# Kernel optimization log

Measured on AMD Instinct MI355X. Metric: run time of the kernel, lower is better.

## Reference

```python
import jax, jax.numpy as jnp
import numpy as np


def _upsample_bilinear_ac(img, out_h, out_w):
    # bilinear upsample with align_corners=True (matches nn.Upsample(..., align_corners=True))
    B, C, H, W = img.shape
    ys = jnp.linspace(0.0, H - 1.0, out_h)
    xs = jnp.linspace(0.0, W - 1.0, out_w)
    y0 = jnp.floor(ys).astype(jnp.int32)
    y1 = jnp.clip(y0 + 1, 0, H - 1)
    x0 = jnp.floor(xs).astype(jnp.int32)
    x1 = jnp.clip(x0 + 1, 0, W - 1)
    wy = (ys - y0).astype(img.dtype)
    wx = (xs - x0).astype(img.dtype)
    top = img[:, :, y0, :] * (1 - wy)[None, None, :, None] + img[:, :, y1, :] * wy[None, None, :, None]
    out = top[:, :, :, x0] * (1 - wx)[None, None, None, :] + top[:, :, :, x1] * wx[None, None, None, :]
    return out


def setup_inputs() -> dict:
    key = jax.random.key(0)
    ks = jax.random.split(key, 10)
    B, Cin, H, W = 4, 1024, 128, 128
    Cy, Hy, Wy = 2, 64, 64
    x = jax.random.normal(ks[0], (B, Cin, H, W), jnp.float32)
    y = jax.random.normal(ks[1], (B, Cy, Hy, Wy), jnp.float32)
    s = 0.5
    wq = jax.random.normal(ks[2], (Cy, Cy), jnp.float32) * s
    bq = jax.random.normal(ks[3], (Cy,), jnp.float32) * 0.1
    wk = jax.random.normal(ks[4], (Cy, Cy), jnp.float32) * s
    bk = jax.random.normal(ks[5], (Cy,), jnp.float32) * 0.1
    wv = jax.random.normal(ks[6], (Cy, Cy), jnp.float32) * s
    bv = jax.random.normal(ks[7], (Cy,), jnp.float32) * 0.1
    gamma = jnp.full((1,), 0.5, jnp.float32)  # torch init is 0; use 0.5 so the attention branch is active
    conv_w = jax.random.normal(ks[8], (Cy, Cin, 3, 3), jnp.float32) * (1.0 / np.sqrt(Cin * 9))
    conv_b = jnp.zeros((Cy,), jnp.float32)
    bn_scale = jnp.ones((Cy,), jnp.float32)
    bn_bias = jnp.zeros((Cy,), jnp.float32)
    bn_mean = jnp.zeros((Cy,), jnp.float32)
    bn_var = jax.random.uniform(ks[9], (Cy,), jnp.float32, 0.5, 1.5)
    return {"x": x, "y": y, "wq": wq, "bq": bq, "wk": wk, "bk": bk, "wv": wv, "bv": bv,
            "gamma": gamma, "conv_w": conv_w, "conv_b": conv_b,
            "bn_scale": bn_scale, "bn_bias": bn_bias, "bn_mean": bn_mean, "bn_var": bn_var}


def reference(x, y, wq, bq, wk, bk, wv, bv, gamma, conv_w, conv_b, bn_scale, bn_bias, bn_mean, bn_var):
    B, Cy, Hy, Wy = y.shape
    N = Hy * Wy
    h, w = x.shape[2], x.shape[3]
    # 1x1 convs on y = channel matmuls
    q = jnp.einsum('oc,bchw->bohw', wq, y) + bq[None, :, None, None]
    k = jnp.einsum('oc,bchw->bohw', wk, y) + bk[None, :, None, None]
    v = jnp.einsum('oc,bchw->bohw', wv, y) + bv[None, :, None, None]
    qf = q.reshape(B, Cy, N)
    kf = k.reshape(B, Cy, N)
    vf = v.reshape(B, Cy, N)
    # energy[b,i,j] = sum_c q[b,c,i] * k[b,c,j]; softmax over j
    energy = jnp.einsum('bci,bcj->bij', qf, kf)
    attn = jax.nn.softmax(energy, axis=-1)
    # out[b,c,i] = sum_j v[b,c,j] * attn[b,i,j]
    out = jnp.einsum('bcj,bij->bci', vf, attn).reshape(B, Cy, Hy, Wy)
    y1 = gamma * out + y
    y1_up = _upsample_bilinear_ac(y1, h, w)
    y_up = _upsample_bilinear_ac(y, h, w)
    # Conv2dBnRelu: 3x3 conv pad 1, BN (eval mode), ReLU
    xc = jax.lax.conv_general_dilated(x, conv_w, (1, 1), ((1, 1), (1, 1)),
                                      dimension_numbers=('NCHW', 'OIHW', 'NCHW'))
    xc = xc + conv_b[None, :, None, None]
    inv = (bn_scale / jnp.sqrt(bn_var + 1e-5))[None, :, None, None]
    xc = (xc - bn_mean[None, :, None, None]) * inv + bn_bias[None, :, None, None]
    xc = jax.nn.relu(xc)
    return y_up + xc * y1_up
```

## Files before the change

kernel.cpp:

```cpp
#include <hip/hip_runtime.h>

#define NATT 4096

__global__ __launch_bounds__(256) void attn_y1_kernel(
    const float* __restrict__ y,
    const float* __restrict__ wq, const float* __restrict__ bq,
    const float* __restrict__ wk, const float* __restrict__ bk,
    const float* __restrict__ wv, const float* __restrict__ bv,
    const float* __restrict__ gammaP,
    float* __restrict__ y1out)
{
    __shared__ float kv[16 * 1024];
    const int tid = threadIdx.x;
    const int blk = blockIdx.x;
    const int b   = blk >> 6;
    const int i0  = (blk & 63) << 6;
    const float* yb = y + (size_t)b * 2 * NATT;

    const float wk00 = wk[0], wk01 = wk[1], wk10 = wk[2], wk11 = wk[3];
    const float wv00 = wv[0], wv01 = wv[1], wv10 = wv[2], wv11 = wv[3];
    const float bk0 = bk[0], bk1 = bk[1], bv0 = bv[0], bv1 = bv[1];

#pragma unroll
    for (int t = 0; t < 16; ++t) {
        int j = tid + (t << 8);
        float ya  = yb[j];
        float ybv = yb[NATT + j];
        float k0 = wk00 * ya + wk01 * ybv + bk0;
        float k1 = wk10 * ya + wk11 * ybv + bk1;
        float v0 = wv00 * ya + wv01 * ybv + bv0;
        float v1 = wv10 * ya + wv11 * ybv + bv1;
        int addr = (t << 10) + (((tid + t) & 255) << 2);
        *(float4*)&kv[addr] = make_float4(k0, k1, v0, v1);
    }
    __syncthreads();

    const int jseg = tid & 15;
    const int ii   = tid >> 4;

    const float wq00 = wq[0], wq01 = wq[1], wq10 = wq[2], wq11 = wq[3];
    const float bq0 = bq[0], bq1 = bq[1];

    float q0[4], q1[4];
#pragma unroll
    for (int m = 0; m < 4; ++m) {
        int i = i0 + ii + (m << 4);
        float ya = yb[i], ybv = yb[NATT + i];
        q0[m] = wq00 * ya + wq01 * ybv + bq0;
        q1[m] = wq10 * ya + wq11 * ybv + bq1;
    }

    float s[4]  = {0.f, 0.f, 0.f, 0.f};
    float a0[4] = {0.f, 0.f, 0.f, 0.f};
    float a1[4] = {0.f, 0.f, 0.f, 0.f};
    const int base = jseg << 10;
#pragma unroll 4
    for (int jj = 0; jj < 256; ++jj) {
        float4 kvv = *(const float4*)&kv[base + (((jj + jseg) & 255) << 2)];
#pragma unroll
        for (int m = 0; m < 4; ++m) {
            float e = fmaf(q0[m], kvv.x, q1[m] * kvv.y);
            float p = __expf(e);
            s[m] += p;
            a0[m] = fmaf(p, kvv.z, a0[m]);
            a1[m] = fmaf(p, kvv.w, a1[m]);
        }
    }
#pragma unroll
    for (int d = 1; d < 16; d <<= 1) {
#pragma unroll
        for (int m = 0; m < 4; ++m) {
            s[m]  += __shfl_xor(s[m],  d, 64);
            a0[m] += __shfl_xor(a0[m], d, 64);
            a1[m] += __shfl_xor(a1[m], d, 64);
        }
    }
    if (jseg == 0) {
        float g = gammaP[0];
#pragma unroll
        for (int m = 0; m < 4; ++m) {
            int i = i0 + ii + (m << 4);
            float o0 = a0[m] / s[m];
            float o1 = a1[m] / s[m];
            y1out[(size_t)b * 2 * NATT + i]        = g * o0 + yb[i];
            y1out[(size_t)b * 2 * NATT + NATT + i] = g * o1 + yb[NATT + i];
        }
    }
}

__global__ __launch_bounds__(256) void conv_part_kernel(
    const float* __restrict__ x, const float* __restrict__ cw,
    float* __restrict__ part)
{
    const int bid = blockIdx.x;
    const int g = bid & 31;
    const int s = (bid >> 5) & 3;
    const int b = bid >> 7;
    const int tid = threadIdx.x;
    const int col = tid & 31;
    const int rg  = tid >> 5;
    const int rowbase = (s << 5) + (rg << 2);
    const int lane = tid & 63;

    const float* xp  = x + (((size_t)(b * 1024 + g * 32)) << 14) + (col << 2);
    const float* w0p = cw + (size_t)g * 32 * 9;
    const float* w1p = w0p + 9216;

    float4 acc[4][2];
#pragma unroll
    for (int i = 0; i < 4; ++i)
#pragma unroll
        for (int oc = 0; oc < 2; ++oc)
            acc[i][oc] = make_float4(0.f, 0.f, 0.f, 0.f);

    float4 cur[6], nxt[6];
    auto loadrows = [&](int c, float4* dst) {
        const float* xc = xp + ((size_t)c << 14);
#pragma unroll
        for (int k = 0; k < 6; ++k) {
            int gr  = rowbase - 1 + k;
            int grc = gr < 0 ? 0 : (gr > 127 ? 127 : gr);
            float4 v = *(const float4*)(xc + (grc << 7));
            if (gr < 0 || gr > 127) v = make_float4(0.f, 0.f, 0.f, 0.f);
            dst[k] = v;
        }
    };

    loadrows(0, cur);
#pragma unroll 1
    for (int ci = 0; ci < 32; ++ci) {
        if (ci < 31) loadrows(ci + 1, nxt);
        const float* wa = w0p + ci * 9;
        const float* wb = w1p + ci * 9;
        float W[2][9];
#pragma unroll
        for (int t = 0; t < 9; ++t) { W[0][t] = wa[t]; W[1][t] = wb[t]; }

        float lf[6], rf[6];
#pragma unroll
        for (int k = 0; k < 6; ++k) {
            float lv = __shfl(cur[k].w, (lane - 1) & 63, 64);
            float rv = __shfl(cur[k].x, (lane + 1) & 63, 64);
            lf[k] = (col == 0)  ? 0.f : lv;
            rf[k] = (col == 31) ? 0.f : rv;
        }
#pragma unroll
        for (int i = 0; i < 4; ++i) {
#pragma unroll
            for (int dr = 0; dr < 3; ++dr) {
                const int k = i + dr;
                const float f0 = lf[k],  f1 = cur[k].x, f2 = cur[k].y,
                            f3 = cur[k].z, f4 = cur[k].w, f5 = rf[k];
#pragma unroll
                for (int oc = 0; oc < 2; ++oc) {
                    const float w0 = W[oc][dr * 3 + 0];
                    const float w1 = W[oc][dr * 3 + 1];
                    const float w2 = W[oc][dr * 3 + 2];
                    acc[i][oc].x = fmaf(w0, f0, fmaf(w1, f1, fmaf(w2, f2, acc[i][oc].x)));
                    acc[i][oc].y = fmaf(w0, f1, fmaf(w1, f2, fmaf(w2, f3, acc[i][oc].y)));
                    acc[i][oc].z = fmaf(w0, f2, fmaf(w1, f3, fmaf(w2, f4, acc[i][oc].z)));
                    acc[i][oc].w = fmaf(w0, f3, fmaf(w1, f4, fmaf(w2, f5, acc[i][oc].w)));
                }
            }
        }
        if (ci < 31) {
#pragma unroll
            for (int k = 0; k < 6; ++k) cur[k] = nxt[k];
        }
    }

    float* pb = part + (((size_t)(g * 4 + b) * 2) << 14) + (col << 2);
#pragma unroll
    for (int i = 0; i < 4; ++i) {
        int orow = rowbase + i;
        *(float4*)(pb + (orow << 7))             = acc[i][0];
        *(float4*)(pb + (1 << 14) + (orow << 7)) = acc[i][1];
    }
}

__global__ __launch_bounds__(256) void combine_kernel(
    const float* __restrict__ part,
    const float* __restrict__ y,
    const float* __restrict__ y1w,
    const float* __restrict__ convb,
    const float* __restrict__ bns, const float* __restrict__ bnb,
    const float* __restrict__ bnm, const float* __restrict__ bnv,
    float* __restrict__ out)
{
    const int idx = blockIdx.x * 256 + threadIdx.x;
    const int w  = idx & 127;
    const int h  = (idx >> 7) & 127;
    const int oc = (idx >> 14) & 1;
    const int b  = idx >> 15;

    float conv = 0.f;
#pragma unroll
    for (int g = 0; g < 32; ++g)
        conv += part[(size_t)g * 131072 + idx];
    conv += convb[oc];

    float inv = bns[oc] * rsqrtf(bnv[oc] + 1e-5f);
    float xc  = (conv - bnm[oc]) * inv + bnb[oc];
    xc = fmaxf(xc, 0.f);

    float sy = (float)(h * 63) * (1.0f / 127.0f);
    int   y0i = (int)sy;
    float wy  = sy - (float)y0i;
    int   y1i = y0i < 63 ? y0i + 1 : 63;
    float sx = (float)(w * 63) * (1.0f / 127.0f);
    int   x0i = (int)sx;
    float wx  = sx - (float)x0i;
    int   x1i = x0i < 63 ? x0i + 1 : 63;

    const size_t cb = ((size_t)(b * 2 + oc)) << 12;
    const float* yc = y   + cb;
    const float* zc = y1w + cb;
    const int i00 = y0i * 64 + x0i, i01 = y0i * 64 + x1i;
    const int i10 = y1i * 64 + x0i, i11 = y1i * 64 + x1i;
    float yup = (1.f - wy) * ((1.f - wx) * yc[i00] + wx * yc[i01])
              +        wy  * ((1.f - wx) * yc[i10] + wx * yc[i11]);
    float zup = (1.f - wy) * ((1.f - wx) * zc[i00] + wx * zc[i01])
              +        wy  * ((1.f - wx) * zc[i10] + wx * zc[i11]);

    out[idx] = yup + xc * zup;
}

extern "C" void kernel_launch(void* const* d_in, const int* in_sizes, int n_in,
                              void* d_out, int out_size, void* d_ws, size_t ws_size,
                              hipStream_t stream)
{
    const float* x     = (const float*)d_in[0];
    const float* y     = (const float*)d_in[1];
    const float* wq    = (const float*)d_in[2];
    const float* bq    = (const float*)d_in[3];
    const float* wk    = (const float*)d_in[4];
    const float* bk    = (const float*)d_in[5];
    const float* wv    = (const float*)d_in[6];
    const float* bv    = (const float*)d_in[7];
    const float* gamma = (const float*)d_in[8];
    const float* cw    = (const float*)d_in[9];
    const float* cb    = (const float*)d_in[10];
    const float* bns   = (const float*)d_in[11];
    const float* bnb   = (const float*)d_in[12];
    const float* bnm   = (const float*)d_in[13];
    const float* bnv   = (const float*)d_in[14];

    float* out  = (float*)d_out;
    float* part = (float*)d_ws;
    float* y1w  = (float*)((char*)d_ws + (size_t)32 * 131072 * 4);

    hipLaunchKernelGGL(conv_part_kernel, dim3(512), dim3(256), 0, stream, x, cw, part);
    hipLaunchKernelGGL(attn_y1_kernel,   dim3(256), dim3(256), 0, stream,
                       y, wq, bq, wk, bk, wv, bv, gamma, y1w);
    hipLaunchKernelGGL(combine_kernel,   dim3(512), dim3(256), 0, stream,
                       part, y, y1w, cb, bns, bnb, bnm, bnv, out);
}
```

Measured before the change: 404.4 us.

## Fuse conv-partial and attention into one launch, halve channel groups, vectorize combine

The conv partial-sum kernel and the attention kernel are merged into one launch: the first 256 blocks compute conv partials over 64-channel groups (16 groups instead of 32), and the remaining 256 blocks compute attention. The two independent stages can then run concurrently on the GPU, and one launch is removed. The combine kernel reads half as many partial buffers and processes four outputs per thread with float4 loads and stores. In exchange, each conv block runs twice as long, and conv blocks now carry the 64KB shared allocation declared for the attention path, which may limit occupancy.

```diff
diff --git a/kernel.cpp b/kernel.cpp
--- a/kernel.cpp
+++ b/kernel.cpp
@@ -1,180 +1,179 @@
 #include <hip/hip_runtime.h>
 
 #define NATT 4096
-
-__global__ __launch_bounds__(256) void attn_y1_kernel(
+#define NCONV 256
+
+__global__ __launch_bounds__(256) void fused_conv_attn_kernel(
+    const float* __restrict__ x, const float* __restrict__ cw,
     const float* __restrict__ y,
     const float* __restrict__ wq, const float* __restrict__ bq,
     const float* __restrict__ wk, const float* __restrict__ bk,
     const float* __restrict__ wv, const float* __restrict__ bv,
     const float* __restrict__ gammaP,
-    float* __restrict__ y1out)
+    float* __restrict__ part, float* __restrict__ y1out)
 {
     __shared__ float kv[16 * 1024];
+    const int bid = blockIdx.x;
     const int tid = threadIdx.x;
-    const int blk = blockIdx.x;
-    const int b   = blk >> 6;
-    const int i0  = (blk & 63) << 6;
-    const float* yb = y + (size_t)b * 2 * NATT;
-
-    const float wk00 = wk[0], wk01 = wk[1], wk10 = wk[2], wk11 = wk[3];
-    const float wv00 = wv[0], wv01 = wv[1], wv10 = wv[2], wv11 = wv[3];
-    const float bk0 = bk[0], bk1 = bk[1], bv0 = bv[0], bv1 = bv[1];
-
-#pragma unroll
-    for (int t = 0; t < 16; ++t) {
-        int j = tid + (t << 8);
-        float ya  = yb[j];
-        float ybv = yb[NATT + j];
-        float k0 = wk00 * ya + wk01 * ybv + bk0;
-        float k1 = wk10 * ya + wk11 * ybv + bk1;
-        float v0 = wv00 * ya + wv01 * ybv + bv0;
-        float v1 = wv10 * ya + wv11 * ybv + bv1;
-        int addr = (t << 10) + (((tid + t) & 255) << 2);
-        *(float4*)&kv[addr] = make_float4(k0, k1, v0, v1);
-    }
-    __syncthreads();
-
-    const int jseg = tid & 15;
-    const int ii   = tid >> 4;
-
-    const float wq00 = wq[0], wq01 = wq[1], wq10 = wq[2], wq11 = wq[3];
-    const float bq0 = bq[0], bq1 = bq[1];
-
-    float q0[4], q1[4];
-#pragma unroll
-    for (int m = 0; m < 4; ++m) {
-        int i = i0 + ii + (m << 4);
-        float ya = yb[i], ybv = yb[NATT + i];
-        q0[m] = wq00 * ya + wq01 * ybv + bq0;
-        q1[m] = wq10 * ya + wq11 * ybv + bq1;
-    }
-
-    float s[4]  = {0.f, 0.f, 0.f, 0.f};
-    float a0[4] = {0.f, 0.f, 0.f, 0.f};
-    float a1[4] = {0.f, 0.f, 0.f, 0.f};
-    const int base = jseg << 10;
-#pragma unroll 4
-    for (int jj = 0; jj < 256; ++jj) {
-        float4 kvv = *(const float4*)&kv[base + (((jj + jseg) & 255) << 2)];
-#pragma unroll
-        for (int m = 0; m < 4; ++m) {
-            float e = fmaf(q0[m], kvv.x, q1[m] * kvv.y);
-            float p = __expf(e);
-            s[m] += p;
-            a0[m] = fmaf(p, kvv.z, a0[m]);
-            a1[m] = fmaf(p, kvv.w, a1[m]);
-        }
-    }
-#pragma unroll
-    for (int d = 1; d < 16; d <<= 1) {
-#pragma unroll
-        for (int m = 0; m < 4; ++m) {
-            s[m]  += __shfl_xor(s[m],  d, 64);
-            a0[m] += __shfl_xor(a0[m], d, 64);
-            a1[m] += __shfl_xor(a1[m], d, 64);
-        }
-    }
-    if (jseg == 0) {
-        float g = gammaP[0];
+
+    if (bid < NCONV) {
+        const int g = bid & 15;
+        const int s = (bid >> 4) & 3;
+        const int b = bid >> 6;
+        const int col = tid & 31;
+        const int rg  = tid >> 5;
+        const int rowbase = (s << 5) + (rg << 2);
+        const int lane = tid & 63;
+
+        const float* xp  = x + (((size_t)(b * 1024 + g * 64)) << 14) + (col << 2);
+        const float* w0p = cw + (size_t)g * 64 * 9;
+        const float* w1p = w0p + 9216;
+
+        float4 acc[4][2];
+#pragma unroll
+        for (int i = 0; i < 4; ++i)
+#pragma unroll
+            for (int oc = 0; oc < 2; ++oc)
+                acc[i][oc] = make_float4(0.f, 0.f, 0.f, 0.f);
+
+        float4 cur[6], nxt[6];
+        auto loadrows = [&](int c, float4* dst) {
+            const float* xc = xp + ((size_t)c << 14);
+#pragma unroll
+            for (int k = 0; k < 6; ++k) {
+                int gr  = rowbase - 1 + k;
+                int grc = gr < 0 ? 0 : (gr > 127 ? 127 : gr);
+                float4 v = *(const float4*)(xc + (grc << 7));
+                if (gr < 0 || gr > 127) v = make_float4(0.f, 0.f, 0.f, 0.f);
+                dst[k] = v;
+            }
+        };
+
+        loadrows(0, cur);
+#pragma unroll 1
+        for (int ci = 0; ci < 64; ++ci) {
+            if (ci < 63) loadrows(ci + 1, nxt);
+            const float* wa = w0p + ci * 9;
+            const float* wb = w1p + ci * 9;
+            float W[2][9];
+#pragma unroll
+            for (int t = 0; t < 9; ++t) { W[0][t] = wa[t]; W[1][t] = wb[t]; }
+
+            float lf[6], rf[6];
+#pragma unroll
+            for (int k = 0; k < 6; ++k) {
+                float lv = __shfl(cur[k].w, (lane - 1) & 63, 64);
+                float rv = __shfl(cur[k].x, (lane + 1) & 63, 64);
+                lf[k] = (col == 0)  ? 0.f : lv;
+                rf[k] = (col == 31) ? 0.f : rv;
+            }
+#pragma unroll
+            for (int i = 0; i < 4; ++i) {
+#pragma unroll
+                for (int dr = 0; dr < 3; ++dr) {
+                    const int k = i + dr;
+                    const float f0 = lf[k],  f1 = cur[k].x, f2 = cur[k].y,
+                                f3 = cur[k].z, f4 = cur[k].w, f5 = rf[k];
+#pragma unroll
+                    for (int oc = 0; oc < 2; ++oc) {
+                        const float w0 = W[oc][dr * 3 + 0];
+                        const float w1 = W[oc][dr * 3 + 1];
+                        const float w2 = W[oc][dr * 3 + 2];
+                        acc[i][oc].x = fmaf(w0, f0, fmaf(w1, f1, fmaf(w2, f2, acc[i][oc].x)));
+                        acc[i][oc].y = fmaf(w0, f1, fmaf(w1, f2, fmaf(w2, f3, acc[i][oc].y)));
+                        acc[i][oc].z = fmaf(w0, f2, fmaf(w1, f3, fmaf(w2, f4, acc[i][oc].z)));
+                        acc[i][oc].w = fmaf(w0, f3, fmaf(w1, f4, fmaf(w2, f5, acc[i][oc].w)));
+                    }
+                }
+            }
+            if (ci < 63) {
+#pragma unroll
+                for (int k = 0; k < 6; ++k) cur[k] = nxt[k];
+            }
+        }
+
+        float* pb = part + (size_t)g * 131072 + (((size_t)b * 2) << 14) + (col << 2);
+#pragma unroll
+        for (int i = 0; i < 4; ++i) {
+            int orow = rowbase + i;
+            *(float4*)(pb + (orow << 7))             = acc[i][0];
+            *(float4*)(pb + (1 << 14) + (orow << 7)) = acc[i][1];
+        }
+    } else {
+        const int blk = bid - NCONV;
+        const int b   = blk >> 6;
+        const int i0  = (blk & 63) << 6;
+        const float* yb = y + (size_t)b * 2 * NATT;
+
+        const float wk00 = wk[0], wk01 = wk[1], wk10 = wk[2], wk11 = wk[3];
+        const float wv00 = wv[0], wv01 = wv[1], wv10 = wv[2], wv11 = wv[3];
+        const float bk0 = bk[0], bk1 = bk[1], bv0 = bv[0], bv1 = bv[1];
+
+#pragma unroll
+        for (int t = 0; t < 16; ++t) {
+            int j = tid + (t << 8);
+            float ya  = yb[j];
+            float ybv = yb[NATT + j];
+            float k0 = wk00 * ya + wk01 * ybv + bk0;
+            float k1 = wk10 * ya + wk11 * ybv + bk1;
+            float v0 = wv00 * ya + wv01 * ybv + bv0;
+            float v1 = wv10 * ya + wv11 * ybv + bv1;
+            int addr = (t << 10) + (((tid + t) & 255) << 2);
+            *(float4*)&kv[addr] = make_float4(k0, k1, v0, v1);
+        }
+        __syncthreads();
+
+        const int jseg = tid & 15;
+        const int ii   = tid >> 4;
+
+        const float wq00 = wq[0], wq01 = wq[1], wq10 = wq[2], wq11 = wq[3];
+        const float bq0 = bq[0], bq1 = bq[1];
+
+        float q0[4], q1[4];
 #pragma unroll
         for (int m = 0; m < 4; ++m) {
             int i = i0 + ii + (m << 4);
-            float o0 = a0[m] / s[m];
-            float o1 = a1[m] / s[m];
-            y1out[(size_t)b * 2 * NATT + i]        = g * o0 + yb[i];
-            y1out[(size_t)b * 2 * NATT + NATT + i] = g * o1 + yb[NATT + i];
-        }
-    }
-}
-
-__global__ __launch_bounds__(256) void conv_part_kernel(
-    const float* __restrict__ x, const float* __restrict__ cw,
-    float* __restrict__ part)
-{
-    const int bid = blockIdx.x;
-    const int g = bid & 31;
-    const int s = (bid >> 5) & 3;
-    const int b = bid >> 7;
-    const int tid = threadIdx.x;
-    const int col = tid & 31;
-    const int rg  = tid >> 5;
-    const int rowbase = (s << 5) + (rg << 2);
-    const int lane = tid & 63;
-
-    const float* xp  = x + (((size_t)(b * 1024 + g * 32)) << 14) + (col << 2);
-    const float* w0p = cw + (size_t)g * 32 * 9;
-    const float* w1p = w0p + 9216;
-
-    float4 acc[4][2];
-#pragma unroll
-    for (int i = 0; i < 4; ++i)
-#pragma unroll
-        for (int oc = 0; oc < 2; ++oc)
-            acc[i][oc] = make_float4(0.f, 0.f, 0.f, 0.f);
-
-    float4 cur[6], nxt[6];
-    auto loadrows = [&](int c, float4* dst) {
-        const float* xc = xp + ((size_t)c << 14);
-#pragma unroll
-        for (int k = 0; k < 6; ++k) {
-            int gr  = rowbase - 1 + k;
-            int grc = gr < 0 ? 0 : (gr > 127 ? 127 : gr);
-            float4 v = *(const float4*)(xc + (grc << 7));
-            if (gr < 0 || gr > 127) v = make_float4(0.f, 0.f, 0.f, 0.f);
-            dst[k] = v;
-        }
-    };
-
-    loadrows(0, cur);
-#pragma unroll 1
-    for (int ci = 0; ci < 32; ++ci) {
-        if (ci < 31) loadrows(ci + 1, nxt);
-        const float* wa = w0p + ci * 9;
-        const float* wb = w1p + ci * 9;
-        float W[2][9];
-#pragma unroll
-        for (int t = 0; t < 9; ++t) { W[0][t] = wa[t]; W[1][t] = wb[t]; }
-
-        float lf[6], rf[6];
-#pragma unroll
-        for (int k = 0; k < 6; ++k) {
-            float lv = __shfl(cur[k].w, (lane - 1) & 63, 64);
-            float rv = __shfl(cur[k].x, (lane + 1) & 63, 64);
-            lf[k] = (col == 0)  ? 0.f : lv;
-            rf[k] = (col == 31) ? 0.f : rv;
-        }
-#pragma unroll
-        for (int i = 0; i < 4; ++i) {
-#pragma unroll
-            for (int dr = 0; dr < 3; ++dr) {
-                const int k = i + dr;
-                const float f0 = lf[k],  f1 = cur[k].x, f2 = cur[k].y,
-                            f3 = cur[k].z, f4 = cur[k].w, f5 = rf[k];
-#pragma unroll
-                for (int oc = 0; oc < 2; ++oc) {
-                    const float w0 = W[oc][dr * 3 + 0];
-                    const float w1 = W[oc][dr * 3 + 1];
-                    const float w2 = W[oc][dr * 3 + 2];
-                    acc[i][oc].x = fmaf(w0, f0, fmaf(w1, f1, fmaf(w2, f2, acc[i][oc].x)));
-                    acc[i][oc].y = fmaf(w0, f1, fmaf(w1, f2, fmaf(w2, f3, acc[i][oc].y)));
-                    acc[i][oc].z = fmaf(w0, f2, fmaf(w1, f3, fmaf(w2, f4, acc[i][oc].z)));
-                    acc[i][oc].w = fmaf(w0, f3, fmaf(w1, f4, fmaf(w2, f5, acc[i][oc].w)));
-                }
-            }
-        }
-        if (ci < 31) {
-#pragma unroll
-            for (int k = 0; k < 6; ++k) cur[k] = nxt[k];
-        }
-    }
-
-    float* pb = part + (((size_t)(g * 4 + b) * 2) << 14) + (col << 2);
-#pragma unroll
-    for (int i = 0; i < 4; ++i) {
-        int orow = rowbase + i;
-        *(float4*)(pb + (orow << 7))             = acc[i][0];
-        *(float4*)(pb + (1 << 14) + (orow << 7)) = acc[i][1];
+            float ya = yb[i], ybv = yb[NATT + i];
+            q0[m] = wq00 * ya + wq01 * ybv + bq0;
+            q1[m] = wq10 * ya + wq11 * ybv + bq1;
+        }
+
+        float s[4]  = {0.f, 0.f, 0.f, 0.f};
+        float a0[4] = {0.f, 0.f, 0.f, 0.f};
+        float a1[4] = {0.f, 0.f, 0.f, 0.f};
+        const int base = jseg << 10;
+#pragma unroll 4
+        for (int jj = 0; jj < 256; ++jj) {
+            float4 kvv = *(const float4*)&kv[base + (((jj + jseg) & 255) << 2)];
+#pragma unroll
+            for (int m = 0; m < 4; ++m) {
+                float e = fmaf(q0[m], kvv.x, q1[m] * kvv.y);
+                float p = __expf(e);
+                s[m] += p;
+                a0[m] = fmaf(p, kvv.z, a0[m]);
+                a1[m] = fmaf(p, kvv.w, a1[m]);
+            }
+        }
+#pragma unroll
+        for (int d = 1; d < 16; d <<= 1) {
+#pragma unroll
+            for (int m = 0; m < 4; ++m) {
+                s[m]  += __shfl_xor(s[m],  d, 64);
+                a0[m] += __shfl_xor(a0[m], d, 64);
+                a1[m] += __shfl_xor(a1[m], d, 64);
+            }
+        }
+        if (jseg == 0) {
+            float g = gammaP[0];
+#pragma unroll
+            for (int m = 0; m < 4; ++m) {
+                int i = i0 + ii + (m << 4);
+                float o0 = a0[m] / s[m];
+                float o1 = a1[m] / s[m];
+                y1out[(size_t)b * 2 * NATT + i]        = g * o0 + yb[i];
+                y1out[(size_t)b * 2 * NATT + NATT + i] = g * o1 + yb[NATT + i];
+            }
+        }
     }
 }
 
@@ -187,42 +186,50 @@
     const float* __restrict__ bnm, const float* __restrict__ bnv,
     float* __restrict__ out)
 {
-    const int idx = blockIdx.x * 256 + threadIdx.x;
-    const int w  = idx & 127;
-    const int h  = (idx >> 7) & 127;
-    const int oc = (idx >> 14) & 1;
-    const int b  = idx >> 15;
-
-    float conv = 0.f;
-#pragma unroll
-    for (int g = 0; g < 32; ++g)
-        conv += part[(size_t)g * 131072 + idx];
-    conv += convb[oc];
-
-    float inv = bns[oc] * rsqrtf(bnv[oc] + 1e-5f);
-    float xc  = (conv - bnm[oc]) * inv + bnb[oc];
-    xc = fmaxf(xc, 0.f);
-
-    float sy = (float)(h * 63) * (1.0f / 127.0f);
-    int   y0i = (int)sy;
-    float wy  = sy - (float)y0i;
-    int   y1i = y0i < 63 ? y0i + 1 : 63;
-    float sx = (float)(w * 63) * (1.0f / 127.0f);
-    int   x0i = (int)sx;
-    float wx  = sx - (float)x0i;
-    int   x1i = x0i < 63 ? x0i + 1 : 63;
+    const int t   = blockIdx.x * 256 + threadIdx.x;
+    const int idx = t << 2;
+    const int w0c = idx & 127;
+    const int h   = (idx >> 7) & 127;
+    const int oc  = (idx >> 14) & 1;
+    const int b   = idx >> 15;
+
+    const float* pbase = part + (((size_t)(b * 2 + oc)) << 14) + (h << 7) + w0c;
+    float cv[4] = {0.f, 0.f, 0.f, 0.f};
+#pragma unroll
+    for (int g = 0; g < 16; ++g) {
+        float4 p = *(const float4*)(pbase + (size_t)g * 131072);
+        cv[0] += p.x; cv[1] += p.y; cv[2] += p.z; cv[3] += p.w;
+    }
+    const float inv = bns[oc] * rsqrtf(bnv[oc] + 1e-5f);
+    const float aff = (convb[oc] - bnm[oc]) * inv + bnb[oc];
+
+    const float sy = (float)(h * 63) * (1.0f / 127.0f);
+    const int   y0i = (int)sy;
+    const float wy  = sy - (float)y0i;
+    const int   y1i = y0i < 63 ? y0i + 1 : 63;
 
     const size_t cb = ((size_t)(b * 2 + oc)) << 12;
     const float* yc = y   + cb;
     const float* zc = y1w + cb;
-    const int i00 = y0i * 64 + x0i, i01 = y0i * 64 + x1i;
-    const int i10 = y1i * 64 + x0i, i11 = y1i * 64 + x1i;
-    float yup = (1.f - wy) * ((1.f - wx) * yc[i00] + wx * yc[i01])
-              +        wy  * ((1.f - wx) * yc[i10] + wx * yc[i11]);
-    float zup = (1.f - wy) * ((1.f - wx) * zc[i00] + wx * zc[i01])
-              +        wy  * ((1.f - wx) * zc[i10] + wx * zc[i11]);
-
-    out[idx] = yup + xc * zup;
+
+    float res[4];
+#pragma unroll
+    for (int e = 0; e < 4; ++e) {
+        float xc = fmaxf(fmaf(cv[e], inv, aff), 0.f);
+        int w = w0c + e;
+        float sx = (float)(w * 63) * (1.0f / 127.0f);
+        int   x0i = (int)sx;
+        float wx  = sx - (float)x0i;
+        int   x1i = x0i < 63 ? x0i + 1 : 63;
+        int i00 = y0i * 64 + x0i, i01 = y0i * 64 + x1i;
+        int i10 = y1i * 64 + x0i, i11 = y1i * 64 + x1i;
+        float yup = (1.f - wy) * ((1.f - wx) * yc[i00] + wx * yc[i01])
+                  +        wy  * ((1.f - wx) * yc[i10] + wx * yc[i11]);
+        float zup = (1.f - wy) * ((1.f - wx) * zc[i00] + wx * zc[i01])
+                  +        wy  * ((1.f - wx) * zc[i10] + wx * zc[i11]);
+        res[e] = yup + xc * zup;
+    }
+    *(float4*)&out[idx] = make_float4(res[0], res[1], res[2], res[3]);
 }
 
 extern "C" void kernel_launch(void* const* d_in, const int* in_sizes, int n_in,
@@ -247,11 +254,10 @@
 
     float* out  = (float*)d_out;
     float* part = (float*)d_ws;
-    float* y1w  = (float*)((char*)d_ws + (size_t)32 * 131072 * 4);
-
-    hipLaunchKernelGGL(conv_part_kernel, dim3(512), dim3(256), 0, stream, x, cw, part);
-    hipLaunchKernelGGL(attn_y1_kernel,   dim3(256), dim3(256), 0, stream,
-                       y, wq, bq, wk, bk, wv, bv, gamma, y1w);
-    hipLaunchKernelGGL(combine_kernel,   dim3(512), dim3(256), 0, stream,
+    float* y1w  = (float*)((char*)d_ws + (size_t)16 * 131072 * 4);
+
+    hipLaunchKernelGGL(fused_conv_attn_kernel, dim3(512), dim3(256), 0, stream,
+                       x, cw, y, wq, bq, wk, bk, wv, bv, gamma, part, y1w);
+    hipLaunchKernelGGL(combine_kernel, dim3(128), dim3(256), 0, stream,
                        part, y, y1w, cb, bns, bnb, bnm, bnv, out);
 }
```

After: 393.8 us. 1.03x faster.
